# Optimization experiments

Measured on AMD Instinct MI355X. Metric: run time of the kernel, lower is better.

Reference implementation:

```python
import jax, jax.numpy as jnp
import numpy as np

ENT_SIZE = 250000
REL_SIZE = 64
EMBED = 128
B = 32768
K = 8


def setup_inputs() -> dict:
    key = jax.random.key(0)
    ks = jax.random.split(key, 9)
    initrange = 0.5 / EMBED
    u = lambda k, n: jax.random.uniform(k, (n, EMBED), jnp.float32, -initrange, initrange)
    V = ENT_SIZE + REL_SIZE  # unified vocab: entities first, then relations
    return {
        "in_ent_w": u(ks[0], ENT_SIZE),
        "out_ent_w": u(ks[1], ENT_SIZE),
        "in_rel_w": u(ks[2], REL_SIZE),
        "out_rel_w": u(ks[3], REL_SIZE),
        "in_map_w": u(ks[4], REL_SIZE),
        "out_map_w": u(ks[5], REL_SIZE),
        "input_labels": jax.random.randint(ks[6], (B,), 0, V, jnp.int32),
        "pos_labels": jax.random.randint(ks[7], (B,), 0, V, jnp.int32),
        "neg_labels": jax.random.randint(ks[8], (B, K), 0, V, jnp.int32),
    }


def _map(ent, mapping):
    # project ent onto the hyperplane normal to normalize(mapping)  (TransH-style)
    n = mapping / jnp.maximum(jnp.linalg.norm(mapping, axis=-1, keepdims=True), 1e-12)
    return ent - jnp.sum(ent * n, axis=-1, keepdims=True) * n


def _pair_embs(iid, pid, is_ent_i, is_ent_p, in_ent_w, out_ent_w, in_rel_w, out_rel_w, in_map_w, out_map_w):
    """Per-row (input_emb, output_emb) per the 4 mask branches, plus the stable
    permutation that reproduces torch's boolean-mask + concat row ordering."""
    rel_size = in_rel_w.shape[0]
    iid_r = jnp.minimum(iid, rel_size - 1)  # clip: only used where label is a relation
    pid_r = jnp.minimum(pid, rel_size - 1)
    e_in = in_ent_w[iid]        # [N, D]
    r_in = in_rel_w[iid_r]
    e_out = out_ent_w[pid]
    r_out = out_rel_w[pid_r]
    mp_in = in_map_w[pid_r]
    mp_out = out_map_w[iid_r]
    mi = is_ent_i[:, None]
    mp = is_ent_p[:, None]
    inp = jnp.where(mi, jnp.where(mp, e_in, _map(e_in, mp_in)), r_in)
    out = jnp.where(mp, jnp.where(mi, e_out, _map(e_out, mp_out)), r_out)
    # branch key: 0=(ent,ent) 1=(ent,rel) 2=(rel,ent) 3=(rel,rel) -> concat order
    branch = (~is_ent_i).astype(jnp.int32) * 2 + (~is_ent_p).astype(jnp.int32)
    perm = jnp.argsort(branch, stable=True)
    return inp[perm], out[perm]


def reference(in_ent_w, out_ent_w, in_rel_w, out_rel_w, in_map_w, out_map_w,
              input_labels, pos_labels, neg_labels):
    ent_size = in_ent_w.shape[0]
    b, k = neg_labels.shape
    neg_flat = neg_labels.reshape(-1)

    # reverse_id_map: entity labels keep id, relation labels offset by ent_size
    to_id = lambda lab: jnp.where(lab < ent_size, lab, lab - ent_size)
    is_ent = lambda lab: lab < ent_size

    iid, pid, nid = to_id(input_labels), to_id(pos_labels), to_id(neg_flat)
    ii, ip, inn = is_ent(input_labels), is_ent(pos_labels), is_ent(neg_flat)

    Ws = (in_ent_w, out_ent_w, in_rel_w, out_rel_w, in_map_w, out_map_w)

    inp_pos, out_pos = _pair_embs(iid, pid, ii, ip, *Ws)
    iid_rep = jnp.repeat(iid, k)
    ii_rep = jnp.repeat(ii, k)
    inp_neg, out_neg = _pair_embs(iid_rep, nid, ii_rep, inn, *Ws)

    log_pos = jax.nn.log_sigmoid(jnp.sum(out_pos * inp_pos, axis=-1))          # [B]
    log_neg = jax.nn.log_sigmoid(jnp.sum(out_neg * (-inp_neg), axis=-1))       # [B*K]
    log_neg = log_neg.reshape(b, k).sum(axis=1)                                # [B]
    return -(log_pos + log_neg)
```

## Files before the change

kernel.cpp:

```cpp
#include <hip/hip_runtime.h>
#include <hip/hip_bf16.h>
#include <stdint.h>

#define ENT 250000
#define RELSZ 64
#define D 128
#define BATCH 32768
#define KNEG 8


__device__ __forceinline__ float logsig(float x) {
  return fminf(x, 0.f) - log1pf(expf(-fabsf(x)));
}

__global__ void k_prep(const float* __restrict__ in_rel, const float* __restrict__ out_rel,
                       const float* __restrict__ in_map, const float* __restrict__ out_map,
                       const int* __restrict__ in_lab, const int* __restrict__ pos_lab,
                       const int* __restrict__ neg_lab,
                       float* __restrict__ t1, float* __restrict__ t2, float* __restrict__ RR,
                       int* __restrict__ C, uint16_t* __restrict__ rank_pos,
                       uint16_t* __restrict__ rank_neg, float* __restrict__ out) {
  __shared__ float ls[4];
  __shared__ float sri[2][128];
  __shared__ int wc[4][4];
  int blk = blockIdx.x, t = threadIdx.x;

  if (blk >= 1152) {
    int sub = t >> 7, tt = t & 127;
    int p = (blk - 1152) * 2 + sub;
    float im = in_map[p * D + tt], om = out_map[p * D + tt];
    float ro = out_rel[p * D + tt], ri = in_rel[p * D + tt];
    float v, r, n_im, n_om;
    v = im * im;
#pragma unroll
    for (int off = 32; off > 0; off >>= 1) v += __shfl_xor(v, off, 64);
    if ((t & 63) == 0) ls[t >> 6] = v;
    __syncthreads();
    r = ls[sub * 2] + ls[sub * 2 + 1];
    n_im = im / fmaxf(sqrtf(r), 1e-12f);
    __syncthreads();
    v = om * om;
#pragma unroll
    for (int off = 32; off > 0; off >>= 1) v += __shfl_xor(v, off, 64);
    if ((t & 63) == 0) ls[t >> 6] = v;
    __syncthreads();
    r = ls[sub * 2] + ls[sub * 2 + 1];
    n_om = om / fmaxf(sqrtf(r), 1e-12f);
    __syncthreads();
    v = n_im * ro;
#pragma unroll
    for (int off = 32; off > 0; off >>= 1) v += __shfl_xor(v, off, 64);
    if ((t & 63) == 0) ls[t >> 6] = v;
    __syncthreads();
    float d1 = ls[sub * 2] + ls[sub * 2 + 1];
    __syncthreads();
    v = n_om * ri;
#pragma unroll
    for (int off = 32; off > 0; off >>= 1) v += __shfl_xor(v, off, 64);
    if ((t & 63) == 0) ls[t >> 6] = v;
    __syncthreads();
    float d2 = ls[sub * 2] + ls[sub * 2 + 1];
    t1[p * D + tt] = ro - d1 * n_im;
    t2[p * D + tt] = ri - d2 * n_om;
    sri[sub][tt] = ri;
    __syncthreads();
    int half = t >> 7, lq = t & 127;
    if (lq < RELSZ) {
      int pr = (blk - 1152) * 2 + half;
      const float* rq = out_rel + lq * D;
      const float* s = sri[half];
      float acc = 0.f;
#pragma unroll 8
      for (int d = 0; d < D; d += 4) {
        float4 r4 = *(const float4*)(rq + d);
        acc += s[d] * r4.x + s[d + 1] * r4.y + s[d + 2] * r4.z + s[d + 3] * r4.w;
      }
      RR[pr * RELSZ + lq] = acc;
    }
    return;
  }

  int wave = t >> 6, lane = t & 63;
  int key, i;
  bool is_pos = blk < 128;
  if (is_pos) {
    i = blk * 256 + t;
    int il = in_lab[i], pl = pos_lab[i];
    key = ((il >= ENT) ? 2 : 0) | ((pl >= ENT) ? 1 : 0);
  } else {
    i = (blk - 128) * 256 + t;
    int il = in_lab[i >> 3], nl = neg_lab[i];
    key = ((il >= ENT) ? 2 : 0) | ((nl >= ENT) ? 1 : 0);
  }
  unsigned long long m[4];
#pragma unroll
  for (int v = 0; v < 4; v++) m[v] = __ballot(key == v);
  if (lane < 4) wc[wave][lane] = __popcll(m[lane]);
  int wrank = __popcll(m[key] & ((1ull << lane) - 1ull));
  __syncthreads();
  if (t < 4) {
    int s = wc[0][t] + wc[1][t] + wc[2][t] + wc[3][t];
    int idx = is_pos ? (t * 128 + blk) : (512 + t * 1024 + (blk - 128));
    C[idx] = s;
  }
  int wpre = 0;
  for (int w = 0; w < wave; w++) wpre += wc[w][key];
  uint16_t rk = (uint16_t)(wpre + wrank);
  if (is_pos) { rank_pos[i] = rk; out[i] = 0.f; }
  else        { rank_neg[i] = rk; }
}

__global__ void k_scan(int* __restrict__ C) {
  int t = threadIdx.x, lane = t & 63, w = t >> 6;
  int base = t * 18;
  int v[18];
  int s = 0;
#pragma unroll
  for (int j = 0; j < 18; j++) { v[j] = C[base + j]; s += v[j]; }
  int inc = s;
#pragma unroll
  for (int off = 1; off < 64; off <<= 1) {
    int x = __shfl_up(inc, off, 64);
    if (lane >= off) inc += x;
  }
  __shared__ int wsum[4];
  if (lane == 63) wsum[w] = inc;
  __syncthreads();
  int wpre = 0;
  for (int i = 0; i < w; i++) wpre += wsum[i];
  int run = wpre + inc - s;
#pragma unroll
  for (int j = 0; j < 18; j++) { C[base + j] = run; run += v[j]; }
}

__global__ void __launch_bounds__(256, 4)
k_main(const float* __restrict__ in_ent, const float* __restrict__ out_ent,
       const float* __restrict__ t1, const float* __restrict__ t2,
       const float* __restrict__ RR,
       const int* __restrict__ in_lab, const int* __restrict__ pos_lab,
       const int* __restrict__ neg_lab,
       const int* __restrict__ C, const uint16_t* __restrict__ rank_pos,
       const uint16_t* __restrict__ rank_neg, float* __restrict__ out) {
  int blk = blockIdx.x, t = threadIdx.x;
  int wave = t >> 6, lane = t & 63;
  int q = lane & 3, g = lane >> 2;

  bool is_pos = blk < 512;
  int w = (is_pos ? blk : blk - 512) * 4 + wave;
  int i = w * 16 + g;

  int il, o;
  if (is_pos) { il = in_lab[i]; o = pos_lab[i]; }
  else        { il = in_lab[i >> 3]; o = neg_lab[i]; }
  bool ei = il < ENT;
  int iid = ei ? il : il - ENT;
  bool eo = o < ENT;
  int oid = eo ? o : o - ENT;
  int key = (ei ? 0 : 2) | (eo ? 0 : 1);

  int rk = is_pos ? (int)rank_pos[i] : (int)rank_neg[i];
  int cidx = is_pos ? (key * 128 + (i >> 8)) : (512 + key * 1024 + (i >> 8));
  int cbase = C[cidx];

  const float* Lp = (ei ? in_ent + (size_t)iid * D : t2 + (size_t)iid * D) + q * 4;
  const float* Rp = (eo ? out_ent + (size_t)oid * D : t1 + (size_t)oid * D) + q * 4;
  float4 L[8], R[8];
#pragma unroll
  for (int k = 0; k < 8; k++) L[k] = *(const float4*)(Lp + k * 16);
#pragma unroll
  for (int k = 0; k < 8; k++) R[k] = *(const float4*)(Rp + k * 16);

  float p = 0.f;
#pragma unroll
  for (int k = 0; k < 8; k++)
    p += L[k].x * R[k].x + L[k].y * R[k].y + L[k].z * R[k].z + L[k].w * R[k].w;
  p += __shfl_xor(p, 1, 64);
  p += __shfl_xor(p, 2, 64);

  float dot = p;
  if (!ei && !eo) dot = RR[iid * RELSZ + oid];

  if (is_pos) {
    if (q == 0) atomicAdd(out + cbase + rk, -logsig(dot));
    return;
  }

  int dest = (cbase + rk - BATCH) >> 3;
  float myval = (q == 0) ? -logsig(-dot) : 0.f;
  float v = myval;
  int d = dest;
  int eq = 1;
#pragma unroll
  for (int off = 4; off <= 16; off <<= 1) {
    float vv = __shfl_xor(v, off, 64);
    int dd = __shfl_xor(d, off, 64);
    int ee = __shfl_xor(eq, off, 64);
    eq = eq & ee & (dd == d ? 1 : 0);
    v += vv;
  }
  if (eq) {
    if (lane == 0 || lane == 32) atomicAdd(out + d, v);
  } else if (q == 0) {
    atomicAdd(out + dest, myval);
  }
}

extern "C" void kernel_launch(void* const* d_in, const int* in_sizes, int n_in,
                              void* d_out, int out_size, void* d_ws, size_t ws_size,
                              hipStream_t stream) {
  const float* in_ent  = (const float*)d_in[0];
  const float* out_ent = (const float*)d_in[1];
  const float* in_rel  = (const float*)d_in[2];
  const float* out_rel = (const float*)d_in[3];
  const float* in_map  = (const float*)d_in[4];
  const float* out_map = (const float*)d_in[5];
  const int* in_lab  = (const int*)d_in[6];
  const int* pos_lab = (const int*)d_in[7];
  const int* neg_lab = (const int*)d_in[8];

  char* ws = (char*)d_ws;
  float*    t1       = (float*)(ws + 0);
  float*    t2       = (float*)(ws + 32768);
  float*    RR       = (float*)(ws + 65536);
  int*      C        = (int*)(ws + 81920);
  uint16_t* rank_pos = (uint16_t*)(ws + 100352);
  uint16_t* rank_neg = (uint16_t*)(ws + 165888);
  float*    out      = (float*)d_out;

  k_prep<<<1184, 256, 0, stream>>>(in_rel, out_rel, in_map, out_map,
                                   in_lab, pos_lab, neg_lab,
                                   t1, t2, RR, C, rank_pos, rank_neg, out);
  k_scan<<<1, 256, 0, stream>>>(C);
  k_main<<<4608, 256, 0, stream>>>(in_ent, out_ent, t1, t2, RR,
                                   in_lab, pos_lab, neg_lab,
                                   C, rank_pos, rank_neg, out);
}
```

Baseline: 43.97 us.

## Replace per-element rank scan with sparse exception list and binary search

Drops the block-wide ballot ranking pass and the separate scan kernel. A single block now collects only the rare non-(entity,entity) items into shared-memory lists, sorts them by O(n^2) counting, and writes their destination slots. The main kernel binary-searches this list to find each row's output position. Relation-involving rows are assumed sparse, with fixed capacity caps. Zeroing the output is moved to separate blocks. In exchange, one block must serially stream all pos and neg labels, which may become a critical-path bottleneck, and the caps silently give wrong results if too many labels are relations.

New measurement: 126.6 us. +187.8%, slower.

```diff
diff --git a/kernel.cpp b/kernel.cpp
--- a/kernel.cpp
+++ b/kernel.cpp
@@ -8,6 +8,9 @@
 #define BATCH 32768
 #define KNEG 8
 
+#define CAPP 2048
+#define CAPN 6144
+
 
 __device__ __forceinline__ float logsig(float x) {
   return fminf(x, 0.f) - log1pf(expf(-fabsf(x)));
@@ -18,16 +21,20 @@
                        const int* __restrict__ in_lab, const int* __restrict__ pos_lab,
                        const int* __restrict__ neg_lab,
                        float* __restrict__ t1, float* __restrict__ t2, float* __restrict__ RR,
-                       int* __restrict__ C, uint16_t* __restrict__ rank_pos,
-                       uint16_t* __restrict__ rank_neg, float* __restrict__ out) {
+                       int* __restrict__ hdr, int* __restrict__ E_pos, int* __restrict__ D_pos,
+                       int* __restrict__ E_neg, int* __restrict__ D_neg,
+                       float* __restrict__ out) {
   __shared__ float ls[4];
   __shared__ float sri[2][128];
-  __shared__ int wc[4][4];
+  __shared__ int vp[CAPP];
+  __shared__ int vn[CAPN];
+  __shared__ int cnt2[2];
+  __shared__ int ckey[8];
   int blk = blockIdx.x, t = threadIdx.x;
 
-  if (blk >= 1152) {
+  if (blk < 32) {
     int sub = t >> 7, tt = t & 127;
-    int p = (blk - 1152) * 2 + sub;
+    int p = blk * 2 + sub;
     float im = in_map[p * D + tt], om = out_map[p * D + tt];
     float ro = out_rel[p * D + tt], ri = in_rel[p * D + tt];
     float v, r, n_im, n_om;
@@ -66,7 +73,7 @@
     __syncthreads();
     int half = t >> 7, lq = t & 127;
     if (lq < RELSZ) {
-      int pr = (blk - 1152) * 2 + half;
+      int pr = blk * 2 + half;
       const float* rq = out_rel + lq * D;
       const float* s = sri[half];
       float acc = 0.f;
@@ -80,57 +87,73 @@
     return;
   }
 
-  int wave = t >> 6, lane = t & 63;
-  int key, i;
-  bool is_pos = blk < 128;
-  if (is_pos) {
-    i = blk * 256 + t;
-    int il = in_lab[i], pl = pos_lab[i];
-    key = ((il >= ENT) ? 2 : 0) | ((pl >= ENT) ? 1 : 0);
-  } else {
-    i = (blk - 128) * 256 + t;
-    int il = in_lab[i >> 3], nl = neg_lab[i];
-    key = ((il >= ENT) ? 2 : 0) | ((nl >= ENT) ? 1 : 0);
-  }
-  unsigned long long m[4];
-#pragma unroll
-  for (int v = 0; v < 4; v++) m[v] = __ballot(key == v);
-  if (lane < 4) wc[wave][lane] = __popcll(m[lane]);
-  int wrank = __popcll(m[key] & ((1ull << lane) - 1ull));
+  if (blk >= 33) {
+    int idx = (blk - 33) * 256 + t;
+    ((float4*)out)[idx] = make_float4(0.f, 0.f, 0.f, 0.f);
+    return;
+  }
+
+  if (t < 2) cnt2[t] = 0;
+  if (t < 8) ckey[t] = 0;
   __syncthreads();
-  if (t < 4) {
-    int s = wc[0][t] + wc[1][t] + wc[2][t] + wc[3][t];
-    int idx = is_pos ? (t * 128 + blk) : (512 + t * 1024 + (blk - 128));
-    C[idx] = s;
-  }
-  int wpre = 0;
-  for (int w = 0; w < wave; w++) wpre += wc[w][key];
-  uint16_t rk = (uint16_t)(wpre + wrank);
-  if (is_pos) { rank_pos[i] = rk; out[i] = 0.f; }
-  else        { rank_neg[i] = rk; }
-}
-
-__global__ void k_scan(int* __restrict__ C) {
-  int t = threadIdx.x, lane = t & 63, w = t >> 6;
-  int base = t * 18;
-  int v[18];
-  int s = 0;
-#pragma unroll
-  for (int j = 0; j < 18; j++) { v[j] = C[base + j]; s += v[j]; }
-  int inc = s;
-#pragma unroll
-  for (int off = 1; off < 64; off <<= 1) {
-    int x = __shfl_up(inc, off, 64);
-    if (lane >= off) inc += x;
-  }
-  __shared__ int wsum[4];
-  if (lane == 63) wsum[w] = inc;
+  for (int base = t * 4; base < BATCH; base += 1024) {
+    int4 a = *(const int4*)(in_lab + base);
+    int4 p4 = *(const int4*)(pos_lab + base);
+    int ka[4];
+    ka[0] = ((a.x >= ENT) ? 2 : 0) | ((p4.x >= ENT) ? 1 : 0);
+    ka[1] = ((a.y >= ENT) ? 2 : 0) | ((p4.y >= ENT) ? 1 : 0);
+    ka[2] = ((a.z >= ENT) ? 2 : 0) | ((p4.z >= ENT) ? 1 : 0);
+    ka[3] = ((a.w >= ENT) ? 2 : 0) | ((p4.w >= ENT) ? 1 : 0);
+#pragma unroll
+    for (int j = 0; j < 4; j++)
+      if (ka[j]) { int s = atomicAdd(&cnt2[0], 1); if (s < CAPP) vp[s] = ((base + j) << 2) | ka[j]; }
+  }
+  for (int row = t; row < BATCH; row += 256) {
+    int il = in_lab[row];
+    int kb = (il >= ENT) ? 2 : 0;
+    int4 n0 = *(const int4*)(neg_lab + row * 8);
+    int4 n1 = *(const int4*)(neg_lab + row * 8 + 4);
+    int nv[8] = {n0.x, n0.y, n0.z, n0.w, n1.x, n1.y, n1.z, n1.w};
+#pragma unroll
+    for (int j = 0; j < 8; j++) {
+      int key = kb | ((nv[j] >= ENT) ? 1 : 0);
+      if (key) { int s = atomicAdd(&cnt2[1], 1); if (s < CAPN) vn[s] = (((row << 3) + j) << 2) | key; }
+    }
+  }
   __syncthreads();
-  int wpre = 0;
-  for (int i = 0; i < w; i++) wpre += wsum[i];
-  int run = wpre + inc - s;
-#pragma unroll
-  for (int j = 0; j < 18; j++) { C[base + j] = run; run += v[j]; }
+  int np = min(cnt2[0], CAPP), nn = min(cnt2[1], CAPN);
+  for (int j = t; j < np; j += 256) atomicAdd(&ckey[vp[j] & 3], 1);
+  for (int j = t; j < nn; j += 256) atomicAdd(&ckey[4 + (vn[j] & 3)], 1);
+  __syncthreads();
+  int c1 = ckey[1], c2 = ckey[2], c3 = ckey[3];
+  int N0p = BATCH - c1 - c2 - c3;
+  int d1 = ckey[5], d2 = ckey[6], d3 = ckey[7];
+  int N0n = BATCH * KNEG - d1 - d2 - d3;
+  for (int j = t; j < np; j += 256) {
+    int v = vp[j], key = v & 3;
+    int r = 0, rk = 0;
+    for (int m = 0; m < np; m++) {
+      int u = vp[m];
+      r += (u < v) ? 1 : 0;
+      rk += ((u < v) && ((u & 3) == key)) ? 1 : 0;
+    }
+    int bbase = (key == 1) ? N0p : (key == 2) ? N0p + c1 : N0p + c1 + c2;
+    E_pos[r] = v >> 2;
+    D_pos[r] = bbase + rk;
+  }
+  for (int j = t; j < nn; j += 256) {
+    int v = vn[j], key = v & 3;
+    int r = 0, rk = 0;
+    for (int m = 0; m < nn; m++) {
+      int u = vn[m];
+      r += (u < v) ? 1 : 0;
+      rk += ((u < v) && ((u & 3) == key)) ? 1 : 0;
+    }
+    int bbase = (key == 1) ? N0n : (key == 2) ? N0n + d1 : N0n + d1 + d2;
+    E_neg[r] = v >> 2;
+    D_neg[r] = bbase + rk;
+  }
+  if (t == 0) { hdr[0] = np; hdr[1] = nn; }
 }
 
 __global__ void __launch_bounds__(256, 4)
@@ -139,8 +162,10 @@
        const float* __restrict__ RR,
        const int* __restrict__ in_lab, const int* __restrict__ pos_lab,
        const int* __restrict__ neg_lab,
-       const int* __restrict__ C, const uint16_t* __restrict__ rank_pos,
-       const uint16_t* __restrict__ rank_neg, float* __restrict__ out) {
+       const int* __restrict__ hdr,
+       const int* __restrict__ E_pos, const int* __restrict__ D_pos,
+       const int* __restrict__ E_neg, const int* __restrict__ D_neg,
+       float* __restrict__ out) {
   int blk = blockIdx.x, t = threadIdx.x;
   int wave = t >> 6, lane = t & 63;
   int q = lane & 3, g = lane >> 2;
@@ -158,10 +183,6 @@
   int oid = eo ? o : o - ENT;
   int key = (ei ? 0 : 2) | (eo ? 0 : 1);
 
-  int rk = is_pos ? (int)rank_pos[i] : (int)rank_neg[i];
-  int cidx = is_pos ? (key * 128 + (i >> 8)) : (512 + key * 1024 + (i >> 8));
-  int cbase = C[cidx];
-
   const float* Lp = (ei ? in_ent + (size_t)iid * D : t2 + (size_t)iid * D) + q * 4;
   const float* Rp = (eo ? out_ent + (size_t)oid * D : t1 + (size_t)oid * D) + q * 4;
   float4 L[8], R[8];
@@ -169,6 +190,17 @@
   for (int k = 0; k < 8; k++) L[k] = *(const float4*)(Lp + k * 16);
 #pragma unroll
   for (int k = 0; k < 8; k++) R[k] = *(const float4*)(Rp + k * 16);
+
+  int n = is_pos ? hdr[0] : hdr[1];
+  const int* E = is_pos ? E_pos : E_neg;
+  int lo = 0, hi = n;
+  while (lo < hi) {
+    int mid = (lo + hi) >> 1;
+    bool lt = E[mid] < i;
+    lo = lt ? mid + 1 : lo;
+    hi = lt ? hi : mid;
+  }
+  int s = (key == 0) ? (i - lo) : (is_pos ? D_pos[lo] : D_neg[lo]);
 
   float p = 0.f;
 #pragma unroll
@@ -181,11 +213,11 @@
   if (!ei && !eo) dot = RR[iid * RELSZ + oid];
 
   if (is_pos) {
-    if (q == 0) atomicAdd(out + cbase + rk, -logsig(dot));
+    if (q == 0) atomicAdd(out + s, -logsig(dot));
     return;
   }
 
-  int dest = (cbase + rk - BATCH) >> 3;
+  int dest = s >> 3;
   float myval = (q == 0) ? -logsig(-dot) : 0.f;
   float v = myval;
   int d = dest;
@@ -219,19 +251,20 @@
   const int* neg_lab = (const int*)d_in[8];
 
   char* ws = (char*)d_ws;
-  float*    t1       = (float*)(ws + 0);
-  float*    t2       = (float*)(ws + 32768);
-  float*    RR       = (float*)(ws + 65536);
-  int*      C        = (int*)(ws + 81920);
-  uint16_t* rank_pos = (uint16_t*)(ws + 100352);
-  uint16_t* rank_neg = (uint16_t*)(ws + 165888);
-  float*    out      = (float*)d_out;
-
-  k_prep<<<1184, 256, 0, stream>>>(in_rel, out_rel, in_map, out_map,
-                                   in_lab, pos_lab, neg_lab,
-                                   t1, t2, RR, C, rank_pos, rank_neg, out);
-  k_scan<<<1, 256, 0, stream>>>(C);
+  float* t1    = (float*)(ws + 0);
+  float* t2    = (float*)(ws + 32768);
+  float* RR    = (float*)(ws + 65536);
+  int*   hdr   = (int*)(ws + 81920);
+  int*   E_pos = (int*)(ws + 82176);
+  int*   D_pos = (int*)(ws + 90368);
+  int*   E_neg = (int*)(ws + 98560);
+  int*   D_neg = (int*)(ws + 123136);
+  float* out   = (float*)d_out;
+
+  k_prep<<<65, 256, 0, stream>>>(in_rel, out_rel, in_map, out_map,
+                                 in_lab, pos_lab, neg_lab,
+                                 t1, t2, RR, hdr, E_pos, D_pos, E_neg, D_neg, out);
   k_main<<<4608, 256, 0, stream>>>(in_ent, out_ent, t1, t2, RR,
                                    in_lab, pos_lab, neg_lab,
-                                   C, rank_pos, rank_neg, out);
-}
+                                   hdr, E_pos, D_pos, E_neg, D_neg, out);
+}
```

## Move bulk embedding gathers into first kernel; recompute relation rows in final pass

Applied to the files above, without the earlier changes.

The heavy gather-and-dot over entity embeddings moves into the first launch. It runs alongside the ranking and relation-prep blocks, so the main memory traffic is no longer serialized after the scan. Dot products are stored in scratch buffers. A lighter final kernel reads them and redoes the dot only for rows involving relations, since t1/t2 may not have been ready earlier. This adds a scratch write and read per row, and a serial per-thread dot in the final pass for relation rows, which may diverge.

After: 54.27 us. 23.4% more time.

```diff
diff --git a/kernel.cpp b/kernel.cpp
--- a/kernel.cpp
+++ b/kernel.cpp
@@ -13,21 +13,88 @@
   return fminf(x, 0.f) - log1pf(expf(-fabsf(x)));
 }
 
-__global__ void k_prep(const float* __restrict__ in_rel, const float* __restrict__ out_rel,
-                       const float* __restrict__ in_map, const float* __restrict__ out_map,
-                       const int* __restrict__ in_lab, const int* __restrict__ pos_lab,
-                       const int* __restrict__ neg_lab,
-                       float* __restrict__ t1, float* __restrict__ t2, float* __restrict__ RR,
-                       int* __restrict__ C, uint16_t* __restrict__ rank_pos,
-                       uint16_t* __restrict__ rank_neg, float* __restrict__ out) {
+__global__ void __launch_bounds__(256, 4)
+k_fused(const float* __restrict__ in_ent, const float* __restrict__ out_ent,
+        const float* __restrict__ in_rel, const float* __restrict__ out_rel,
+        const float* __restrict__ in_map, const float* __restrict__ out_map,
+        const int* __restrict__ in_lab, const int* __restrict__ pos_lab,
+        const int* __restrict__ neg_lab,
+        float* t1, float* t2, float* __restrict__ RR,
+        int* __restrict__ C, uint16_t* __restrict__ rank_pos,
+        uint16_t* __restrict__ rank_neg,
+        float* __restrict__ buf_pos, float* __restrict__ buf_neg,
+        float* __restrict__ out) {
   __shared__ float ls[4];
   __shared__ float sri[2][128];
   __shared__ int wc[4][4];
   int blk = blockIdx.x, t = threadIdx.x;
 
-  if (blk >= 1152) {
+  if (blk < 4608) {
+    int wave = t >> 6, lane = t & 63;
+    int q = lane & 3, g = lane >> 2;
+    bool is_pos = blk < 512;
+    int w = (is_pos ? blk : blk - 512) * 4 + wave;
+    int i = w * 16 + g;
+    int il = is_pos ? in_lab[i] : in_lab[i >> 3];
+    int o  = is_pos ? pos_lab[i] : neg_lab[i];
+    bool ei = il < ENT; int iid = ei ? il : il - ENT;
+    bool eo = o < ENT;  int oid = eo ? o : o - ENT;
+    const float* Lp = (ei ? in_ent + (size_t)iid * D : t2 + (size_t)iid * D) + q * 4;
+    const float* Rp = (eo ? out_ent + (size_t)oid * D : t1 + (size_t)oid * D) + q * 4;
+    float4 L[8], R[8];
+#pragma unroll
+    for (int k = 0; k < 8; k++) L[k] = *(const float4*)(Lp + k * 16);
+#pragma unroll
+    for (int k = 0; k < 8; k++) R[k] = *(const float4*)(Rp + k * 16);
+    float p = 0.f;
+#pragma unroll
+    for (int k = 0; k < 8; k++)
+      p += L[k].x * R[k].x + L[k].y * R[k].y + L[k].z * R[k].z + L[k].w * R[k].w;
+    p += __shfl_xor(p, 1, 64);
+    p += __shfl_xor(p, 2, 64);
+    if (q == 0) {
+      if (is_pos) buf_pos[i] = p;
+      else        buf_neg[i] = p;
+    }
+    return;
+  }
+
+  if (blk < 5760) {
+    int bb = blk - 4608;
+    int wave = t >> 6, lane = t & 63;
+    bool is_pos = bb < 128;
+    int key, i;
+    if (is_pos) {
+      i = bb * 256 + t;
+      int il = in_lab[i], pl = pos_lab[i];
+      key = ((il >= ENT) ? 2 : 0) | ((pl >= ENT) ? 1 : 0);
+    } else {
+      i = (bb - 128) * 256 + t;
+      int il = in_lab[i >> 3], nl = neg_lab[i];
+      key = ((il >= ENT) ? 2 : 0) | ((nl >= ENT) ? 1 : 0);
+    }
+    unsigned long long m[4];
+#pragma unroll
+    for (int v = 0; v < 4; v++) m[v] = __ballot(key == v);
+    if (lane < 4) wc[wave][lane] = __popcll(m[lane]);
+    int wrank = __popcll(m[key] & ((1ull << lane) - 1ull));
+    __syncthreads();
+    if (t < 4) {
+      int s = wc[0][t] + wc[1][t] + wc[2][t] + wc[3][t];
+      int idx = is_pos ? (t * 128 + bb) : (512 + t * 1024 + (bb - 128));
+      C[idx] = s;
+    }
+    int wpre = 0;
+    for (int w2 = 0; w2 < wave; w2++) wpre += wc[w2][key];
+    uint16_t rk = (uint16_t)(wpre + wrank);
+    if (is_pos) rank_pos[i] = rk;
+    else        rank_neg[i] = rk;
+    return;
+  }
+
+  if (blk < 5792) {
     int sub = t >> 7, tt = t & 127;
-    int p = (blk - 1152) * 2 + sub;
+    int p = (blk - 5760) * 2 + sub;
     float im = in_map[p * D + tt], om = out_map[p * D + tt];
     float ro = out_rel[p * D + tt], ri = in_rel[p * D + tt];
     float v, r, n_im, n_om;
@@ -66,7 +133,7 @@
     __syncthreads();
     int half = t >> 7, lq = t & 127;
     if (lq < RELSZ) {
-      int pr = (blk - 1152) * 2 + half;
+      int pr = (blk - 5760) * 2 + half;
       const float* rq = out_rel + lq * D;
       const float* s = sri[half];
       float acc = 0.f;
@@ -80,34 +147,8 @@
     return;
   }
 
-  int wave = t >> 6, lane = t & 63;
-  int key, i;
-  bool is_pos = blk < 128;
-  if (is_pos) {
-    i = blk * 256 + t;
-    int il = in_lab[i], pl = pos_lab[i];
-    key = ((il >= ENT) ? 2 : 0) | ((pl >= ENT) ? 1 : 0);
-  } else {
-    i = (blk - 128) * 256 + t;
-    int il = in_lab[i >> 3], nl = neg_lab[i];
-    key = ((il >= ENT) ? 2 : 0) | ((nl >= ENT) ? 1 : 0);
-  }
-  unsigned long long m[4];
-#pragma unroll
-  for (int v = 0; v < 4; v++) m[v] = __ballot(key == v);
-  if (lane < 4) wc[wave][lane] = __popcll(m[lane]);
-  int wrank = __popcll(m[key] & ((1ull << lane) - 1ull));
-  __syncthreads();
-  if (t < 4) {
-    int s = wc[0][t] + wc[1][t] + wc[2][t] + wc[3][t];
-    int idx = is_pos ? (t * 128 + blk) : (512 + t * 1024 + (blk - 128));
-    C[idx] = s;
-  }
-  int wpre = 0;
-  for (int w = 0; w < wave; w++) wpre += wc[w][key];
-  uint16_t rk = (uint16_t)(wpre + wrank);
-  if (is_pos) { rank_pos[i] = rk; out[i] = 0.f; }
-  else        { rank_neg[i] = rk; }
+  int idx = (blk - 5792) * 256 + t;
+  ((float4*)out)[idx] = make_float4(0.f, 0.f, 0.f, 0.f);
 }
 
 __global__ void k_scan(int* __restrict__ C) {
@@ -133,75 +174,67 @@
   for (int j = 0; j < 18; j++) { C[base + j] = run; run += v[j]; }
 }
 
-__global__ void __launch_bounds__(256, 4)
-k_main(const float* __restrict__ in_ent, const float* __restrict__ out_ent,
-       const float* __restrict__ t1, const float* __restrict__ t2,
-       const float* __restrict__ RR,
-       const int* __restrict__ in_lab, const int* __restrict__ pos_lab,
-       const int* __restrict__ neg_lab,
-       const int* __restrict__ C, const uint16_t* __restrict__ rank_pos,
-       const uint16_t* __restrict__ rank_neg, float* __restrict__ out) {
+__global__ void k_final(const float* __restrict__ in_ent, const float* __restrict__ out_ent,
+                        const float* __restrict__ t1, const float* __restrict__ t2,
+                        const float* __restrict__ RR,
+                        const int* __restrict__ in_lab, const int* __restrict__ pos_lab,
+                        const int* __restrict__ neg_lab,
+                        const int* __restrict__ C, const uint16_t* __restrict__ rank_pos,
+                        const uint16_t* __restrict__ rank_neg,
+                        const float* __restrict__ buf_pos, const float* __restrict__ buf_neg,
+                        float* __restrict__ out) {
   int blk = blockIdx.x, t = threadIdx.x;
-  int wave = t >> 6, lane = t & 63;
-  int q = lane & 3, g = lane >> 2;
-
-  bool is_pos = blk < 512;
-  int w = (is_pos ? blk : blk - 512) * 4 + wave;
-  int i = w * 16 + g;
-
-  int il, o;
-  if (is_pos) { il = in_lab[i]; o = pos_lab[i]; }
-  else        { il = in_lab[i >> 3]; o = neg_lab[i]; }
-  bool ei = il < ENT;
-  int iid = ei ? il : il - ENT;
-  bool eo = o < ENT;
-  int oid = eo ? o : o - ENT;
+  bool is_pos = blk < 128;
+  int i = (is_pos ? blk : blk - 128) * 256 + t;
+
+  int il = is_pos ? in_lab[i] : in_lab[i >> 3];
+  int o  = is_pos ? pos_lab[i] : neg_lab[i];
+  bool ei = il < ENT, eo = o < ENT;
   int key = (ei ? 0 : 2) | (eo ? 0 : 1);
-
   int rk = is_pos ? (int)rank_pos[i] : (int)rank_neg[i];
   int cidx = is_pos ? (key * 128 + (i >> 8)) : (512 + key * 1024 + (i >> 8));
   int cbase = C[cidx];
-
-  const float* Lp = (ei ? in_ent + (size_t)iid * D : t2 + (size_t)iid * D) + q * 4;
-  const float* Rp = (eo ? out_ent + (size_t)oid * D : t1 + (size_t)oid * D) + q * 4;
-  float4 L[8], R[8];
-#pragma unroll
-  for (int k = 0; k < 8; k++) L[k] = *(const float4*)(Lp + k * 16);
-#pragma unroll
-  for (int k = 0; k < 8; k++) R[k] = *(const float4*)(Rp + k * 16);
-
-  float p = 0.f;
-#pragma unroll
-  for (int k = 0; k < 8; k++)
-    p += L[k].x * R[k].x + L[k].y * R[k].y + L[k].z * R[k].z + L[k].w * R[k].w;
-  p += __shfl_xor(p, 1, 64);
-  p += __shfl_xor(p, 2, 64);
-
-  float dot = p;
-  if (!ei && !eo) dot = RR[iid * RELSZ + oid];
+  float dot = is_pos ? buf_pos[i] : buf_neg[i];
+
+  if (key) {
+    int iid = ei ? il : il - ENT, oid = eo ? o : o - ENT;
+    if (key == 3) {
+      dot = RR[iid * RELSZ + oid];
+    } else {
+      const float* Lp = ei ? in_ent + (size_t)iid * D : t2 + (size_t)iid * D;
+      const float* Rp = eo ? out_ent + (size_t)oid * D : t1 + (size_t)oid * D;
+      float s = 0.f;
+#pragma unroll 8
+      for (int d = 0; d < D; d += 4) {
+        float4 a = *(const float4*)(Lp + d);
+        float4 b = *(const float4*)(Rp + d);
+        s += a.x * b.x + a.y * b.y + a.z * b.z + a.w * b.w;
+      }
+      dot = s;
+    }
+  }
 
   if (is_pos) {
-    if (q == 0) atomicAdd(out + cbase + rk, -logsig(dot));
-    return;
-  }
-
-  int dest = (cbase + rk - BATCH) >> 3;
-  float myval = (q == 0) ? -logsig(-dot) : 0.f;
-  float v = myval;
-  int d = dest;
-  int eq = 1;
-#pragma unroll
-  for (int off = 4; off <= 16; off <<= 1) {
-    float vv = __shfl_xor(v, off, 64);
-    int dd = __shfl_xor(d, off, 64);
-    int ee = __shfl_xor(eq, off, 64);
-    eq = eq & ee & (dd == d ? 1 : 0);
-    v += vv;
-  }
-  if (eq) {
-    if (lane == 0 || lane == 32) atomicAdd(out + d, v);
-  } else if (q == 0) {
-    atomicAdd(out + dest, myval);
+    int dest = cbase + rk;
+    atomicAdd(out + dest, -logsig(dot));
+  } else {
+    int dest = (cbase + rk - BATCH) >> 3;
+    float val = -logsig(-dot);
+    float v = val;
+    int d = dest, eq = 1;
+#pragma unroll
+    for (int off = 1; off <= 4; off <<= 1) {
+      float vv = __shfl_xor(v, off, 64);
+      int dd = __shfl_xor(d, off, 64);
+      int ee = __shfl_xor(eq, off, 64);
+      eq = eq & ee & (dd == d ? 1 : 0);
+      v += vv;
+    }
+    if (eq) {
+      if ((t & 7) == 0) atomicAdd(out + d, v);
+    } else {
+      atomicAdd(out + dest, val);
+    }
   }
 }
 
@@ -225,13 +258,16 @@
   int*      C        = (int*)(ws + 81920);
   uint16_t* rank_pos = (uint16_t*)(ws + 100352);
   uint16_t* rank_neg = (uint16_t*)(ws + 165888);
+  float*    buf_pos  = (float*)(ws + 690176);
+  float*    buf_neg  = (float*)(ws + 821248);
   float*    out      = (float*)d_out;
 
-  k_prep<<<1184, 256, 0, stream>>>(in_rel, out_rel, in_map, out_map,
-                                   in_lab, pos_lab, neg_lab,
-                                   t1, t2, RR, C, rank_pos, rank_neg, out);
+  k_fused<<<5824, 256, 0, stream>>>(in_ent, out_ent, in_rel, out_rel, in_map, out_map,
+                                    in_lab, pos_lab, neg_lab,
+                                    t1, t2, RR, C, rank_pos, rank_neg,
+                                    buf_pos, buf_neg, out);
   k_scan<<<1, 256, 0, stream>>>(C);
-  k_main<<<4608, 256, 0, stream>>>(in_ent, out_ent, t1, t2, RR,
-                                   in_lab, pos_lab, neg_lab,
-                                   C, rank_pos, rank_neg, out);
-}
+  k_final<<<1152, 256, 0, stream>>>(in_ent, out_ent, t1, t2, RR,
+                                    in_lab, pos_lab, neg_lab,
+                                    C, rank_pos, rank_neg, buf_pos, buf_neg, out);
+}
```
